# Kernel optimization log

Hardware: AMD Instinct MI355X
Metric: run time of the kernel (lower is better)

Reference implementation:

```python
import jax, jax.numpy as jnp
import numpy as np

B, T, F, K = 32, 1500, 512, 31
QBITS = 8
EPS = 1e-5


def fake_quant(x, bits=QBITS):
    """Symmetric per-tensor fake quantization (scale from dynamic max-abs),
    with straight-through estimator so gradients pass through unchanged."""
    qmax = 2.0 ** (bits - 1) - 1.0  # 127 for 8 bits
    scale = jnp.maximum(jnp.max(jnp.abs(x)) / qmax, 1e-8)
    q = jnp.clip(jnp.round(x / scale), -qmax - 1.0, qmax) * scale
    return x + jax.lax.stop_gradient(q - x)


def setup_inputs() -> dict:
    key = jax.random.key(0)
    ks = jax.random.split(key, 5)
    x = jax.random.normal(ks[0], (B, T, F), dtype=jnp.float32)
    W1 = jax.random.normal(ks[1], (2 * F, F), dtype=jnp.float32) * (1.0 / np.sqrt(F))
    b1 = jnp.zeros((2 * F,), jnp.float32)
    dw_w = jax.random.normal(ks[2], (F, 1, K), dtype=jnp.float32) * (1.0 / np.sqrt(K))
    dw_b = jnp.zeros((F,), jnp.float32)
    W2 = jax.random.normal(ks[3], (F, F), dtype=jnp.float32) * (1.0 / np.sqrt(F))
    b2 = jnp.zeros((F,), jnp.float32)
    return {
        "x": x,
        "ln_gamma": jnp.ones((F,), jnp.float32),
        "ln_beta": jnp.zeros((F,), jnp.float32),
        "W1": W1, "b1": b1,
        "dw_w": dw_w, "dw_b": dw_b,
        "bn_gamma": jnp.ones((F,), jnp.float32),
        "bn_beta": jnp.zeros((F,), jnp.float32),
        "W2": W2, "b2": b2,
    }


def _forward(x, ln_gamma, ln_beta, W1, b1, dw_w, dw_b, bn_gamma, bn_beta, W2, b2):
    # LayerNorm over last dim F
    mu = jnp.mean(x, axis=-1, keepdims=True)
    var = jnp.mean(jnp.square(x - mu), axis=-1, keepdims=True)
    t = (x - mu) * jax.lax.rsqrt(var + EPS) * ln_gamma + ln_beta

    # pconv1 in-quant -> quantized pointwise conv1 (Linear F -> 2F) -> out-quant
    t = fake_quant(t)
    t = jnp.einsum("btf,gf->btg", t, fake_quant(W1)) + b1
    t = fake_quant(t)

    # GLU over last dim: [B,T,2F] -> [B,T,F]
    a, g = jnp.split(t, 2, axis=-1)
    t = a * jax.nn.sigmoid(g)

    # depthwise conv on [B,F,T]
    t = jnp.transpose(t, (0, 2, 1))  # [B,F,T]
    t = fake_quant(t)
    t = jax.lax.conv_general_dilated(
        t, fake_quant(dw_w),
        window_strides=(1,),
        padding=[((K - 1) // 2, (K - 1) // 2)],
        feature_group_count=F,
        dimension_numbers=("NCH", "OIH", "NCH"),
    ) + dw_b[None, :, None]
    t = fake_quant(t)

    # BatchNorm1d over channel dim (stats over batch and time), training-style batch stats
    bmu = jnp.mean(t, axis=(0, 2), keepdims=True)
    bvar = jnp.mean(jnp.square(t - bmu), axis=(0, 2), keepdims=True)
    t = (t - bmu) * jax.lax.rsqrt(bvar + EPS) * bn_gamma[None, :, None] + bn_beta[None, :, None]

    t = jnp.transpose(t, (0, 2, 1))  # [B,T,F]
    t = jax.nn.silu(t)

    # pconv2 in-quant -> quantized pointwise conv2 (Linear F -> F) -> out-quant
    t = fake_quant(t)
    t = jnp.einsum("btf,gf->btg", t, fake_quant(W2)) + b2
    t = fake_quant(t)
    return t  # dropout is identity (p=0 / eval)


def reference(x, ln_gamma, ln_beta, W1, b1, dw_w, dw_b, bn_gamma, bn_beta, W2, b2):
    return _forward(x, ln_gamma, ln_beta, W1, b1, dw_w, dw_b, bn_gamma, bn_beta, W2, b2)
```

## Files before the change

### kernel.cpp

```cpp
#include <hip/hip_runtime.h>
#include <stdint.h>

typedef __bf16 bf16;
typedef __bf16   bf16x4 __attribute__((ext_vector_type(4)));
typedef __bf16   bf16x8 __attribute__((ext_vector_type(8)));
typedef short    s16x8  __attribute__((ext_vector_type(8)));
typedef float    fx4    __attribute__((ext_vector_type(4)));

#define NB 32
#define NT 1500
#define NF 512
#define NM (NB*NT)
#define KW 31
#define EPSF 1e-5f

__device__ __forceinline__ float dscale(const float* a) {
  return fmaxf(a[0] * (1.0f/127.0f), 1e-8f);
}
__device__ __forceinline__ float fq_int(float x, float inv_s) {
  return fminf(fmaxf(rintf(x*inv_s), -128.0f), 127.0f);
}
__device__ __forceinline__ void block_amax(float v, float* dst) {
  __shared__ float red[8];
  #pragma unroll
  for (int o = 32; o > 0; o >>= 1) v = fmaxf(v, __shfl_xor(v, o));
  if ((threadIdx.x & 63) == 0) red[threadIdx.x >> 6] = v;
  __syncthreads();
  if (threadIdx.x == 0) {
    int nw = blockDim.x >> 6;
    float m = red[0];
    for (int i = 1; i < nw; i++) m = fmaxf(m, red[i]);
    atomicMax((unsigned int*)dst, __float_as_uint(m));
  }
}

__device__ __forceinline__ float amax_loop(const float* p, long n4, int bid, int gsz) {
  float am = 0.f;
  long i = (long)bid * blockDim.x + threadIdx.x;
  long stride = (long)gsz * blockDim.x;
  for (; i < n4; i += stride) {
    fx4 v = ((const fx4*)p)[i];
    #pragma unroll
    for (int j = 0; j < 4; j++) am = fmaxf(am, fabsf(v[j]));
  }
  return am;
}
__global__ void absmax_w(const float* __restrict__ W1, const float* __restrict__ W2,
                         const float* __restrict__ dwp, float* a) {
  int bx = blockIdx.x;
  float am; float* dst;
  if (bx < 256)      { am = amax_loop(W1,  131072, bx,       256); dst = a + 1; }
  else if (bx < 384) { am = amax_loop(W2,  65536,  bx - 256, 128); dst = a + 2; }
  else               { am = amax_loop(dwp, 3968,   bx - 384, 8);   dst = a + 3; }
  block_amax(am, dst);
}

__global__ void quant_pack(const float* __restrict__ src, bf16* __restrict__ dst,
                           int R, const float* amax) {
  float inv_s = 1.0f / dscale(amax);
  int total = R * 64;
  for (int t = blockIdx.x*blockDim.x + threadIdx.x; t < total; t += gridDim.x*blockDim.x) {
    int r = t >> 6, q8 = t & 63;
    const float* s = src + (size_t)r*512 + q8*8;
    fx4 v0 = *(const fx4*)s, v1 = *(const fx4*)(s+4);
    bf16x8 o;
    #pragma unroll
    for (int j = 0; j < 4; j++) { o[j] = (bf16)fq_int(v0[j], inv_s); o[4+j] = (bf16)fq_int(v1[j], inv_s); }
    int r16 = r >> 4, m16 = r & 15, kb = q8 >> 2, quad = q8 & 3;
    size_t chunk = ((size_t)r16*16 + kb)*64 + quad*16 + m16;
    ((bf16x8*)dst)[chunk] = o;
  }
}

__global__ void quant_deq_f32(float* __restrict__ p, long n4, const float* amax) {
  float s = dscale(amax);
  float inv_s = 1.0f / s;
  long i = (long)blockIdx.x * blockDim.x + threadIdx.x;
  long stride = (long)gridDim.x * blockDim.x;
  for (; i < n4; i += stride) {
    fx4 v = ((fx4*)p)[i];
    fx4 o;
    #pragma unroll
    for (int j = 0; j < 4; j++) o[j] = fq_int(v[j], inv_s) * s;
    ((fx4*)p)[i] = o;
  }
}

__global__ void ln_k(const float* __restrict__ x, const float* __restrict__ g,
                     const float* __restrict__ be, float* __restrict__ t, float* amax) {
  int lane = threadIdx.x & 63;
  int wavesTotal = (gridDim.x * blockDim.x) >> 6;
  int wave = ((blockIdx.x * blockDim.x) + threadIdx.x) >> 6;
  fx4 g0 = ((const fx4*)g)[lane],  g1 = ((const fx4*)g)[lane+64];
  fx4 b0 = ((const fx4*)be)[lane], b1v = ((const fx4*)be)[lane+64];
  float gf[8], bff[8];
  #pragma unroll
  for (int j = 0; j < 4; j++) { gf[j] = g0[j]; gf[4+j] = g1[j]; bff[j] = b0[j]; bff[4+j] = b1v[j]; }
  float am = 0.f;
  for (int row = wave; row < NM; row += wavesTotal) {
    const fx4* xr = (const fx4*)(x + (long)row*NF);
    fx4 x0 = xr[lane], x1 = xr[lane+64];
    float xf[8]; float s = 0.f;
    #pragma unroll
    for (int j = 0; j < 4; j++) { xf[j] = x0[j]; xf[4+j] = x1[j]; }
    #pragma unroll
    for (int j = 0; j < 8; j++) s += xf[j];
    #pragma unroll
    for (int o = 32; o > 0; o >>= 1) s += __shfl_xor(s, o);
    float mu = s * (1.0f/NF);
    float vs = 0.f;
    #pragma unroll
    for (int j = 0; j < 8; j++) { float d = xf[j]-mu; vs += d*d; }
    #pragma unroll
    for (int o = 32; o > 0; o >>= 1) vs += __shfl_xor(vs, o);
    float inv = rsqrtf(vs*(1.0f/NF) + EPSF);
    fx4 o0, o1;
    #pragma unroll
    for (int j = 0; j < 4; j++) {
      float v = (xf[j]-mu)*inv*gf[j] + bff[j];
      am = fmaxf(am, fabsf(v)); o0[j] = v;
    }
    #pragma unroll
    for (int j = 0; j < 4; j++) {
      float v = (xf[4+j]-mu)*inv*gf[4+j] + bff[4+j];
      am = fmaxf(am, fabsf(v)); o1[j] = v;
    }
    ((fx4*)(t + (long)row*NF))[lane]    = o0;
    ((fx4*)(t + (long)row*NF))[lane+64] = o1;
  }
  block_amax(am, amax);
}

template<int NBN>
__global__ __launch_bounds__(256) void gemm_k(
    const bf16* __restrict__ A, const bf16* __restrict__ Bt,
    const float* __restrict__ bias, float* __restrict__ C,
    const float* amaxA, const float* amaxB, float* amaxC) {
  const int N = NBN * 128;
  int id = blockIdx.x;
  int bn = (id >> 3) % NBN;
  int bm = 8 * (id / (8 * NBN)) + (id & 7);
  if (bm >= 375) return;
  int lane = threadIdx.x & 63;
  int w = threadIdx.x >> 6;
  int wm = w >> 1, wn = w & 1;
  int quad = lane >> 4;
  int m16 = lane & 15;

  fx4 acc[4][4];
  #pragma unroll
  for (int i = 0; i < 4; i++)
    #pragma unroll
    for (int j = 0; j < 4; j++) acc[i][j] = fx4{0.f,0.f,0.f,0.f};

  const bf16* pA[4];
  const bf16* pB[4];
  #pragma unroll
  for (int i = 0; i < 4; i++)
    pA[i] = A + ((size_t)(bm*8 + wm*4 + i)*16)*512 + lane*8;
  #pragma unroll
  for (int j = 0; j < 4; j++)
    pB[j] = Bt + ((size_t)(bn*8 + wn*4 + j)*16)*512 + lane*8;

  #pragma unroll
  for (int kb = 0; kb < 16; kb++) {
    s16x8 aF[4], bF[4];
    #pragma unroll
    for (int i = 0; i < 4; i++) aF[i] = *(const s16x8*)(pA[i] + kb*512);
    #pragma unroll
    for (int j = 0; j < 4; j++) bF[j] = *(const s16x8*)(pB[j] + kb*512);
    #pragma unroll
    for (int i = 0; i < 4; i++)
      #pragma unroll
      for (int j = 0; j < 4; j++)
        acc[i][j] = __builtin_amdgcn_mfma_f32_16x16x32_bf16(aF[i], bF[j], acc[i][j], 0, 0, 0);
  }

  float ab = dscale(amaxA) * dscale(amaxB);
  float am = 0.f;
  #pragma unroll
  for (int j = 0; j < 4; j++) {
    int col = bn*128 + wn*64 + j*16 + m16;
    float bv = bias[col];
    #pragma unroll
    for (int i = 0; i < 4; i++) {
      int row0 = bm*128 + wm*64 + i*16 + quad*4;
      #pragma unroll
      for (int rr = 0; rr < 4; rr++) {
        float v = acc[i][j][rr]*ab + bv;
        am = fmaxf(am, fabsf(v));
        C[(long)(row0+rr)*N + col] = v;
      }
    }
  }
  block_amax(am, amaxC);
}

__global__ void glu_k(const float* __restrict__ u, float* __restrict__ v,
                      const float* amaxU, float* amaxV) {
  __shared__ float lds[32][33];
  float s = dscale(amaxU);
  float inv_s = 1.0f / s;
  float am = 0.f;
  int tx = threadIdx.x & 31, ty = threadIdx.x >> 5;
  const int ntile = (NM/32) * (NF/32);
  for (int tile = blockIdx.x; tile < ntile; tile += gridDim.x) {
    int btT = tile % (NM/32), fT = tile / (NM/32);
    int bt0 = btT*32, f0 = fT*32;
    __syncthreads();
    #pragma unroll
    for (int sI = 0; sI < 4; sI++) {
      int rr = ty + sI*8;
      long base = (long)(bt0 + rr)*(2*NF) + f0 + tx;
      float a = fq_int(u[base], inv_s) * s;
      float g = fq_int(u[base + NF], inv_s) * s;
      float val = a * (1.0f/(1.0f + expf(-g)));
      lds[tx][rr] = val;
      am = fmaxf(am, fabsf(val));
    }
    __syncthreads();
    #pragma unroll
    for (int sI = 0; sI < 4; sI++) {
      int f = f0 + ty + sI*8;
      int bt = bt0 + tx;
      int b = bt / NT, t = bt - b*NT;
      v[((long)b*NF + f)*NT + t] = lds[ty + sI*8][tx];
    }
  }
  block_amax(am, amaxV);
}

__global__ void dwconv_k(const float* __restrict__ v, const float* __restrict__ w,
                         const float* __restrict__ wb, float* __restrict__ y,
                         const float* amaxV, const float* amaxW, float* amaxY) {
  __shared__ float z[2][1568];
  __shared__ float wl[2][32];
  float sv = dscale(amaxV); float inv_sv = 1.0f/sv;
  float sw = dscale(amaxW); float inv_sw = 1.0f/sw;
  float am = 0.f;
  const int tid = threadIdx.x;
  const int rr = tid >> 7;
  const int cl = tid & 127;
  const int npairs = (NB*NF)/2;
  for (int pr = blockIdx.x; pr < npairs; pr += gridDim.x) {
    int row0 = pr*2;
    __syncthreads();
    if (tid < 64) {
      int r2 = tid >> 5, k = tid & 31;
      if (k < KW) {
        int f = (row0 + r2) & (NF-1);
        wl[r2][k] = fq_int(w[f*KW + k], inv_sw) * sw;
      }
    }
    if (tid < 128) {
      int r2 = tid >> 6, jj = tid & 63;
      if (jj < 16) z[r2][jj] = 0.f;
      else         z[r2][1500 + jj] = 0.f;
    }
    const fx4* vp = (const fx4*)(v + (long)row0 * NT);
    for (int i = tid; i < 750; i += 256) {
      fx4 q = vp[i];
      int r2 = (i >= 375) ? 1 : 0;
      int ii = i - 375*r2;
      fx4 o;
      #pragma unroll
      for (int j = 0; j < 4; j++) o[j] = fq_int(q[j], inv_sv) * sv;
      *(fx4*)&z[r2][16 + 4*ii] = o;
    }
    __syncthreads();
    float wr[KW];
    #pragma unroll
    for (int k = 0; k < KW; k++) wr[k] = wl[rr][k];
    float bias = wb[(row0 + rr) & (NF-1)];
    long base = (long)(row0 + rr) * NT;
    #pragma unroll
    for (int pass = 0; pass < 3; pass++) {
      int c = cl + pass*128;
      if (c < 375) {
        int t0 = c*4;
        fx4 win[9];
        #pragma unroll
        for (int i = 0; i < 9; i++) win[i] = *(const fx4*)&z[rr][t0 + 4*i];
        float acc0 = bias, acc1 = bias, acc2 = bias, acc3 = bias;
        #pragma unroll
        for (int k = 0; k < KW; k++) {
          float wk = wr[k];
          acc0 += win[(k+1)>>2][(k+1)&3] * wk;
          acc1 += win[(k+2)>>2][(k+2)&3] * wk;
          acc2 += win[(k+3)>>2][(k+3)&3] * wk;
          acc3 += win[(k+4)>>2][(k+4)&3] * wk;
        }
        fx4 o = {acc0, acc1, acc2, acc3};
        #pragma unroll
        for (int j = 0; j < 4; j++) am = fmaxf(am, fabsf(o[j]));
        *(fx4*)&y[base + t0] = o;
      }
    }
  }
  block_amax(am, amaxY);
}

__global__ void bnstats_k(const float* __restrict__ y, const float* amaxY,
                          float* bn_mean, float* bn_rinv) {
  float sy = dscale(amaxY); float inv_sy = 1.0f/sy;
  int f = blockIdx.x;
  int s1 = 0, s2 = 0;
  for (int b = 0; b < NB; b++) {
    const fx4* base = (const fx4*)(y + ((long)b*NF + f)*NT);
    for (int i = threadIdx.x; i < NT/4; i += blockDim.x) {
      fx4 v = base[i];
      #pragma unroll
      for (int j = 0; j < 4; j++) {
        int q = (int)fq_int(v[j], inv_sy);
        s1 += q; s2 += q*q;
      }
    }
  }
  #pragma unroll
  for (int o = 32; o > 0; o >>= 1) { s1 += __shfl_xor(s1, o); s2 += __shfl_xor(s2, o); }
  __shared__ int rs1[4], rs2[4];
  if ((threadIdx.x & 63) == 0) { rs1[threadIdx.x>>6] = s1; rs2[threadIdx.x>>6] = s2; }
  __syncthreads();
  if (threadIdx.x == 0) {
    long long S1 = (long long)rs1[0]+rs1[1]+rs1[2]+rs1[3];
    long long S2 = (long long)rs2[0]+rs2[1]+rs2[2]+rs2[3];
    double s = (double)sy;
    double mean = (double)S1 * s / (double)NM;
    double var  = (double)S2 * s * s / (double)NM - mean*mean;
    bn_mean[f] = (float)mean;
    bn_rinv[f] = rsqrtf((float)var + EPSF);
  }
}

__global__ void bnsilu_k(const float* __restrict__ y, const float* __restrict__ bg,
                         const float* __restrict__ bb, const float* amaxY,
                         const float* bn_mean, const float* bn_rinv,
                         float* __restrict__ p, float* amaxP) {
  __shared__ float lds[32][33];
  float sy = dscale(amaxY); float inv_sy = 1.0f/sy;
  float am = 0.f;
  int tx = threadIdx.x & 31, ty = threadIdx.x >> 5;
  const int TTILES = (NT + 31)/32;
  const int ntile = NB * (NF/32) * TTILES;
  for (int tile = blockIdx.x; tile < ntile; tile += gridDim.x) {
    int b = tile / ((NF/32)*TTILES);
    int rem = tile % ((NF/32)*TTILES);
    int fT = rem / TTILES, tT = rem % TTILES;
    int f0 = fT*32, t0 = tT*32;
    __syncthreads();
    #pragma unroll
    for (int sI = 0; sI < 4; sI++) {
      int f = f0 + ty + sI*8;
      int t = t0 + tx;
      if (t < NT) {
        float zq = fq_int(y[((long)b*NF + f)*NT + t], inv_sy) * sy;
        float val = (zq - bn_mean[f])*bn_rinv[f]*bg[f] + bb[f];
        val = val / (1.0f + expf(-val));
        am = fmaxf(am, fabsf(val));
        lds[tx][ty + sI*8] = val;
      }
    }
    __syncthreads();
    #pragma unroll
    for (int sI = 0; sI < 4; sI++) {
      int t = t0 + ty + sI*8;
      if (t < NT)
        p[((long)b*NT + t)*NF + f0 + tx] = lds[ty + sI*8][tx];
    }
  }
  block_amax(am, amaxP);
}

extern "C" void kernel_launch(void* const* d_in, const int* in_sizes, int n_in,
                              void* d_out, int out_size, void* d_ws, size_t ws_size,
                              hipStream_t stream) {
  const float* x  = (const float*)d_in[0];
  const float* lg = (const float*)d_in[1];
  const float* lb = (const float*)d_in[2];
  const float* W1 = (const float*)d_in[3];
  const float* b1 = (const float*)d_in[4];
  const float* dw = (const float*)d_in[5];
  const float* db = (const float*)d_in[6];
  const float* bg = (const float*)d_in[7];
  const float* bb = (const float*)d_in[8];
  const float* W2 = (const float*)d_in[9];
  const float* b2 = (const float*)d_in[10];
  float* out = (float*)d_out;

  char* ws = (char*)d_ws;
  float* amax    = (float*)ws;
  float* bn_mean = (float*)(ws + 1024);
  float* bn_rinv = (float*)(ws + 4096);
  char* H = ws + 8192;
  float* t_raw = (float*)H;
  float* u_raw = (float*)H;
  bf16*  t_q   = (bf16*)(H + 196608000);
  float* y     = (float*)H;
  float* p_raw = (float*)(H + 98304000);
  bf16*  p_q   = (bf16*)(H + 196608000);
  bf16*  W1q   = (bf16*)(H + 245760000);
  bf16*  W2q   = (bf16*)(H + 246808576);
  float* v = (float*)d_out;
  float* r = (float*)d_out;

  hipMemsetAsync(ws, 0, 8192, stream);

  absmax_w<<<392, 256, 0, stream>>>(W1, W2, dw, amax);
  quant_pack<<<256, 256, 0, stream>>>(W1, W1q, 1024, amax+1);
  quant_pack<<<128, 256, 0, stream>>>(W2, W2q, 512,  amax+2);

  ln_k<<<1536, 256, 0, stream>>>(x, lg, lb, t_raw, amax+0);
  quant_pack<<<4096, 256, 0, stream>>>(t_raw, t_q, NM, amax+0);
  gemm_k<8><<<3008, 256, 0, stream>>>(t_q, W1q, b1, u_raw, amax+0, amax+1, amax+4);
  glu_k<<<4096, 256, 0, stream>>>(u_raw, v, amax+4, amax+5);
  dwconv_k<<<2048, 256, 0, stream>>>(v, dw, db, y, amax+5, amax+3, amax+6);
  bnstats_k<<<512, 256, 0, stream>>>(y, amax+6, bn_mean, bn_rinv);
  bnsilu_k<<<4096, 256, 0, stream>>>(y, bg, bb, amax+6, bn_mean, bn_rinv, p_raw, amax+7);
  quant_pack<<<4096, 256, 0, stream>>>(p_raw, p_q, NM, amax+7);
  gemm_k<4><<<1504, 256, 0, stream>>>(p_q, W2q, b2, r, amax+7, amax+2, amax+8);
  quant_deq_f32<<<2048, 256, 0, stream>>>(out, 24576000/4, amax+8);
}
```

Baseline: 673.6 us.

## Write GEMM1 output transposed and vectorize GEMM epilogue stores

GEMM1 now writes its output in column-major [2F, B*T] layout using 16-byte vector stores. The GLU kernel can then read contiguous rows and write the [B,F,T] layout directly, with no LDS transpose. GEMM2 swaps the MFMA operand order so each lane holds four consecutive output columns, which allows vectorized bias loads and row-major vector stores. This removes scattered scalar stores and the shared-memory transpose, in exchange for strided column writes in GEMM1 that may span many rows of memory.

```diff
diff --git a/kernel.cpp b/kernel.cpp
--- a/kernel.cpp
+++ b/kernel.cpp
@@ -131,7 +131,7 @@
   block_amax(am, amax);
 }
 
-template<int NBN>
+template<int NBN, int MODE>
 __global__ __launch_bounds__(256) void gemm_k(
     const bf16* __restrict__ A, const bf16* __restrict__ Bt,
     const float* __restrict__ bias, float* __restrict__ C,
@@ -172,59 +172,81 @@
     #pragma unroll
     for (int i = 0; i < 4; i++)
       #pragma unroll
-      for (int j = 0; j < 4; j++)
-        acc[i][j] = __builtin_amdgcn_mfma_f32_16x16x32_bf16(aF[i], bF[j], acc[i][j], 0, 0, 0);
+      for (int j = 0; j < 4; j++) {
+        if (MODE == 0)
+          acc[i][j] = __builtin_amdgcn_mfma_f32_16x16x32_bf16(aF[i], bF[j], acc[i][j], 0, 0, 0);
+        else
+          acc[i][j] = __builtin_amdgcn_mfma_f32_16x16x32_bf16(bF[j], aF[i], acc[i][j], 0, 0, 0);
+      }
   }
 
   float ab = dscale(amaxA) * dscale(amaxB);
   float am = 0.f;
-  #pragma unroll
-  for (int j = 0; j < 4; j++) {
-    int col = bn*128 + wn*64 + j*16 + m16;
-    float bv = bias[col];
+  if (MODE == 0) {
+    #pragma unroll
+    for (int j = 0; j < 4; j++) {
+      int col = bn*128 + wn*64 + j*16 + m16;
+      float bv = bias[col];
+      #pragma unroll
+      for (int i = 0; i < 4; i++) {
+        int row0 = bm*128 + wm*64 + i*16 + quad*4;
+        fx4 o;
+        #pragma unroll
+        for (int rr = 0; rr < 4; rr++) {
+          float v = acc[i][j][rr]*ab + bv;
+          am = fmaxf(am, fabsf(v)); o[rr] = v;
+        }
+        *(fx4*)(C + (size_t)col*NM + row0) = o;
+      }
+    }
+  } else {
     #pragma unroll
     for (int i = 0; i < 4; i++) {
-      int row0 = bm*128 + wm*64 + i*16 + quad*4;
-      #pragma unroll
-      for (int rr = 0; rr < 4; rr++) {
-        float v = acc[i][j][rr]*ab + bv;
-        am = fmaxf(am, fabsf(v));
-        C[(long)(row0+rr)*N + col] = v;
+      int m = bm*128 + wm*64 + i*16 + m16;
+      #pragma unroll
+      for (int j = 0; j < 4; j++) {
+        int n0 = bn*128 + wn*64 + j*16 + quad*4;
+        fx4 bv = *(const fx4*)(bias + n0);
+        fx4 o;
+        #pragma unroll
+        for (int rr = 0; rr < 4; rr++) {
+          float v = acc[i][j][rr]*ab + bv[rr];
+          am = fmaxf(am, fabsf(v)); o[rr] = v;
+        }
+        *(fx4*)(C + (size_t)m*N + n0) = o;
       }
     }
   }
   block_amax(am, amaxC);
 }
 
-__global__ void glu_k(const float* __restrict__ u, float* __restrict__ v,
+__global__ void glu_k(const float* __restrict__ uT, float* __restrict__ v,
                       const float* amaxU, float* amaxV) {
-  __shared__ float lds[32][33];
   float s = dscale(amaxU);
   float inv_s = 1.0f / s;
   float am = 0.f;
-  int tx = threadIdx.x & 31, ty = threadIdx.x >> 5;
-  const int ntile = (NM/32) * (NF/32);
-  for (int tile = blockIdx.x; tile < ntile; tile += gridDim.x) {
-    int btT = tile % (NM/32), fT = tile / (NM/32);
-    int bt0 = btT*32, f0 = fT*32;
-    __syncthreads();
-    #pragma unroll
-    for (int sI = 0; sI < 4; sI++) {
-      int rr = ty + sI*8;
-      long base = (long)(bt0 + rr)*(2*NF) + f0 + tx;
-      float a = fq_int(u[base], inv_s) * s;
-      float g = fq_int(u[base + NF], inv_s) * s;
-      float val = a * (1.0f/(1.0f + expf(-g)));
-      lds[tx][rr] = val;
-      am = fmaxf(am, fabsf(val));
-    }
-    __syncthreads();
-    #pragma unroll
-    for (int sI = 0; sI < 4; sI++) {
-      int f = f0 + ty + sI*8;
-      int bt = bt0 + tx;
-      int b = bt / NT, t = bt - b*NT;
-      v[((long)b*NF + f)*NT + t] = lds[ty + sI*8][tx];
+  const int tid = threadIdx.x;
+  const int npairs = (NB*NF)/2;
+  for (int pr = blockIdx.x; pr < npairs; pr += gridDim.x) {
+    int row0 = pr*2;
+    for (int i = tid; i < 750; i += 256) {
+      int r2 = (i >= 375) ? 1 : 0;
+      int c = i - 375*r2;
+      int row = row0 + r2;
+      int b = row >> 9, f = row & (NF-1);
+      long bt = (long)b*NT + c*4;
+      fx4 a = *(const fx4*)(uT + (long)f*NM + bt);
+      fx4 g = *(const fx4*)(uT + (long)(f+NF)*NM + bt);
+      fx4 o;
+      #pragma unroll
+      for (int j = 0; j < 4; j++) {
+        float av = fq_int(a[j], inv_s) * s;
+        float gv = fq_int(g[j], inv_s) * s;
+        float val = av * (1.0f/(1.0f + expf(-gv)));
+        am = fmaxf(am, fabsf(val));
+        o[j] = val;
+      }
+      *(fx4*)(v + (long)row*NT + c*4) = o;
     }
   }
   block_amax(am, amaxV);
@@ -393,7 +415,7 @@
   float* bn_rinv = (float*)(ws + 4096);
   char* H = ws + 8192;
   float* t_raw = (float*)H;
-  float* u_raw = (float*)H;
+  float* uT    = (float*)H;
   bf16*  t_q   = (bf16*)(H + 196608000);
   float* y     = (float*)H;
   float* p_raw = (float*)(H + 98304000);
@@ -411,12 +433,12 @@
 
   ln_k<<<1536, 256, 0, stream>>>(x, lg, lb, t_raw, amax+0);
   quant_pack<<<4096, 256, 0, stream>>>(t_raw, t_q, NM, amax+0);
-  gemm_k<8><<<3008, 256, 0, stream>>>(t_q, W1q, b1, u_raw, amax+0, amax+1, amax+4);
-  glu_k<<<4096, 256, 0, stream>>>(u_raw, v, amax+4, amax+5);
+  gemm_k<8,0><<<3008, 256, 0, stream>>>(t_q, W1q, b1, uT, amax+0, amax+1, amax+4);
+  glu_k<<<4096, 256, 0, stream>>>(uT, v, amax+4, amax+5);
   dwconv_k<<<2048, 256, 0, stream>>>(v, dw, db, y, amax+5, amax+3, amax+6);
   bnstats_k<<<512, 256, 0, stream>>>(y, amax+6, bn_mean, bn_rinv);
   bnsilu_k<<<4096, 256, 0, stream>>>(y, bg, bb, amax+6, bn_mean, bn_rinv, p_raw, amax+7);
   quant_pack<<<4096, 256, 0, stream>>>(p_raw, p_q, NM, amax+7);
-  gemm_k<4><<<1504, 256, 0, stream>>>(p_q, W2q, b2, r, amax+7, amax+2, amax+8);
+  gemm_k<4,1><<<1504, 256, 0, stream>>>(p_q, W2q, b2, r, amax+7, amax+2, amax+8);
   quant_deq_f32<<<2048, 256, 0, stream>>>(out, 24576000/4, amax+8);
 }
```

Result: no change. 677.1 us (+0.5%).
